# Kernel optimization log

Hardware: AMD Instinct MI355X
Metric: run time of the kernel (lower is better)

Reference implementation:

```python
import jax, jax.numpy as jnp
import numpy as np

N_NODES = 100000
N_EDGES = 1600000
N_FEAT = 128
HID = 64
HEADS = 3
CHROM = 21
N_CLASSES = 10
N_GRAPHS = 8
NEG_SLOPE = 0.2
EPS = 1e-5


def _glorot(key, shape):
    fan_in, fan_out = shape[0], shape[-1]
    lim = float(np.sqrt(6.0 / (fan_in + fan_out)))
    return jax.random.uniform(key, shape, jnp.float32, -lim, lim)


def setup_inputs() -> dict:
    key = jax.random.key(0)
    ks = jax.random.split(key, 16)
    x = jax.random.normal(ks[0], (N_NODES, N_FEAT), jnp.float32)
    src = jax.random.randint(ks[1], (N_EDGES,), 0, N_NODES)
    dst = jax.random.randint(ks[2], (N_EDGES,), 0, N_NODES)
    # avoid pre-existing self loops (PyG removes them before adding fresh ones)
    dst = jnp.where(dst == src, (dst + 1) % N_NODES, dst)
    edge_index = jnp.stack([src, dst]).astype(jnp.int64)
    batch = jnp.sort(jax.random.randint(ks[3], (N_NODES,), 0, N_GRAPHS)).astype(jnp.int64)
    d1 = HEADS * HID
    params = {
        # conv1: in 128 -> heads*64, concat=True
        'Wl1': _glorot(ks[4], (N_FEAT, d1)), 'Wr1': _glorot(ks[5], (N_FEAT, d1)),
        'att1': _glorot(ks[6], (HEADS, HID)), 'b1': jnp.zeros((d1,), jnp.float32),
        # batchnorm over 192 features
        'gamma': jnp.ones((d1,), jnp.float32), 'beta': jnp.zeros((d1,), jnp.float32),
        # conv2: in 192 -> 64 (mean over heads)
        'Wl2': _glorot(ks[7], (d1, d1)), 'Wr2': _glorot(ks[8], (d1, d1)),
        'att2': _glorot(ks[9], (HEADS, HID)), 'b2': jnp.zeros((HID,), jnp.float32),
        # conv3: in 64 -> 21 (mean over heads)
        'Wl3': _glorot(ks[10], (HID, HEADS * CHROM)), 'Wr3': _glorot(ks[11], (HID, HEADS * CHROM)),
        'att3': _glorot(ks[12], (HEADS, CHROM)), 'b3': jnp.zeros((CHROM,), jnp.float32),
        # classifier (sized to actual conv2 output width = HID)
        'Wc': _glorot(ks[13], (HID, N_CLASSES)), 'bc': jnp.zeros((N_CLASSES,), jnp.float32),
    }
    return {'x': x, 'edge_index': edge_index, 'batch': batch, **params}


def gatv2(x, src, dst, Wl, Wr, att, bias, concat):
    N = x.shape[0]
    H, D = att.shape
    xl = (x @ Wl).reshape(N, H, D)   # source transform (messages)
    xr = (x @ Wr).reshape(N, H, D)   # target transform
    e = jax.nn.leaky_relu(xl[src] + xr[dst], NEG_SLOPE)          # [E,H,D]
    logits = jnp.einsum('ehd,hd->eh', e, att)                    # [E,H]
    m = jax.ops.segment_max(logits, dst, num_segments=N)         # segment softmax over incoming edges
    ez = jnp.exp(logits - m[dst])
    z = jax.ops.segment_sum(ez, dst, num_segments=N)
    alpha = ez / z[dst]                                          # [E,H]; self-loops guarantee nonempty segments
    out = jax.ops.segment_sum(xl[src] * alpha[:, :, None], dst, num_segments=N)  # [N,H,D]
    out = out.reshape(N, H * D) if concat else out.mean(axis=1)
    return out + bias


def batchnorm(x, gamma, beta):
    mu = x.mean(axis=0)
    var = x.var(axis=0)
    return (x - mu) * jax.lax.rsqrt(var + EPS) * gamma + beta


def reference(x, edge_index, batch, Wl1, Wr1, att1, b1, gamma, beta,
              Wl2, Wr2, att2, b2, Wl3, Wr3, att3, b3, Wc, bc):
    N = x.shape[0]
    loop = jnp.arange(N, dtype=edge_index.dtype)
    src = jnp.concatenate([edge_index[0], loop])
    dst = jnp.concatenate([edge_index[1], loop])

    h = gatv2(x, src, dst, Wl1, Wr1, att1, b1, concat=True)      # [N, 192]
    h = jax.nn.relu(h)
    h = batchnorm(h, gamma, beta)
    h = gatv2(h, src, dst, Wl2, Wr2, att2, b2, concat=False)     # [N, 64]
    color = jax.nn.relu(h)
    color = gatv2(color, src, dst, Wl3, Wr3, att3, b3, concat=False)  # [N, 21]

    # global mean pool over graphs (dropout is eval-mode identity)
    sums = jax.ops.segment_sum(h, batch, num_segments=N_GRAPHS)
    cnt = jax.ops.segment_sum(jnp.ones((N, 1), h.dtype), batch, num_segments=N_GRAPHS)
    pooled = sums / jnp.maximum(cnt, 1.0)                        # [8, 64]
    classif = pooled @ Wc + bc                                   # [8, 10]
    return classif, color
```

## Files before the change

### kernel.cpp

```cpp
#include <hip/hip_runtime.h>
#include <stdint.h>
#include <math.h>

#define N_NODES 100000
#define N_EDGES 1600000
#define ETOT (N_EDGES + N_NODES)
#define NCLS 10
#define NGR 8
#define SCAN_BLOCKS ((N_NODES + 255) / 256)

typedef short v8s __attribute__((ext_vector_type(8)));
typedef float v4f __attribute__((ext_vector_type(4)));
typedef float f4v __attribute__((ext_vector_type(4)));
typedef unsigned short ushort_t;
typedef unsigned short us8 __attribute__((ext_vector_type(8)));
typedef unsigned short us4 __attribute__((ext_vector_type(4)));
typedef _Float16 h2 __attribute__((ext_vector_type(2)));
typedef _Float16 h4 __attribute__((ext_vector_type(4)));
typedef _Float16 h8 __attribute__((ext_vector_type(8)));

__device__ __forceinline__ float b2f(ushort_t u) {
    union { unsigned int i; float f; } v; v.i = ((unsigned int)u) << 16; return v.f;
}
__device__ __forceinline__ ushort_t f2b(float f) {
    union { float f; unsigned int i; } v; v.f = f;
    unsigned int u = v.i;
    unsigned int r = (u + 0x7fffu + ((u >> 16) & 1u)) >> 16;
    return (ushort_t)r;
}
__device__ __forceinline__ ushort_t f2h(float f) {
    union { _Float16 h; ushort_t u; } v; v.h = (_Float16)f; return v.u;
}

#if __has_builtin(__builtin_amdgcn_fdot2)
#define FDOT2(a, b, c) __builtin_amdgcn_fdot2((a), (b), (c), false)
#else
#define FDOT2(a, b, c) ((c) + (float)(a)[0] * (float)(b)[0] + (float)(a)[1] * (float)(b)[1])
#endif
#define SHUF2(v, i, j) __builtin_shufflevector((v), (v), (i), (j))

__device__ __forceinline__ h2 lrelu2(h2 t) {
    const h2 k = {(_Float16)0.2f, (_Float16)0.2f};
    return __builtin_elementwise_max(t, t * k);
}

__global__ void detect_kernel(const int* eidx, const unsigned int* gamma_raw,
                              int* nz, int* isf32) {
    int i = blockIdx.x * 256 + threadIdx.x;
    if (i == 0) *isf32 = (gamma_raw[0] == 0x3F800000u) ? 1 : 0;
    if (eidx[2 * i + 1] != 0) atomicAdd(nz, 1);
}

struct CArgs {
    const void* src[10];
    ushort_t*   dst[10];
    int         len[10];
    int         tohalf[10];
};
__global__ void convert_small(CArgs c, const int* isf32) {
    int seg = blockIdx.x;
    int f32 = *isf32;
    int th = c.tohalf[seg];
    for (int i = threadIdx.x; i < c.len[seg]; i += 256) {
        float v = f32 ? ((const float*)c.src[seg])[i] : b2f(((const ushort_t*)c.src[seg])[i]);
        c.dst[seg][i] = th ? f2h(v) : f2b(v);
    }
}

struct TArgs {
    const void* W[6];
    ushort_t*   Wt[6];
    int K[6], Nn[6], Kp[6], Np[6];
    int bstart[7];
};
__global__ void transpose_all(TArgs t, const int* isf32) {
    int b = blockIdx.x;
    int seg = 0;
    while (seg < 5 && b >= t.bstart[seg + 1]) seg++;
    int i = (b - t.bstart[seg]) * 256 + threadIdx.x;
    int Kp = t.Kp[seg];
    if (i >= t.Np[seg] * Kp) return;
    int n = i / Kp, k = i - n * Kp;
    ushort_t v = 0;
    if (n < t.Nn[seg] && k < t.K[seg]) {
        long idx = (long)k * t.Nn[seg] + n;
        v = (*isf32) ? f2b(((const float*)t.W[seg])[idx]) : ((const ushort_t*)t.W[seg])[idx];
    }
    t.Wt[seg][i] = v;
}

__global__ void hist_kernel(const int* eidx, const int* nz, int* counts) {
    long i = (long)blockIdx.x * 256 + threadIdx.x;
    if (i >= ETOT) return;
    int w64 = (*nz == 0);
    int d;
    if (i < N_EDGES) d = w64 ? eidx[2 * (N_EDGES + i)] : eidx[N_EDGES + i];
    else             d = (int)(i - N_EDGES);
    if ((unsigned)d >= N_NODES) d = 0;
    atomicAdd(&counts[d], 1);
}

__global__ void scan_part(const int* counts, int* blocksum) {
    __shared__ int red[256];
    int i = blockIdx.x * 256 + threadIdx.x;
    int v = (i < N_NODES) ? counts[i] : 0;
    red[threadIdx.x] = v;
    __syncthreads();
    for (int off = 128; off > 0; off >>= 1) {
        if (threadIdx.x < off) red[threadIdx.x] += red[threadIdx.x + off];
        __syncthreads();
    }
    if (threadIdx.x == 0) blocksum[blockIdx.x] = red[0];
}

__global__ void scan_top(int* blocksum) {
    __shared__ int part[512];
    int t = threadIdx.x;
    int v = (t < SCAN_BLOCKS) ? blocksum[t] : 0;
    part[t] = v;
    __syncthreads();
    for (int off = 1; off < 512; off <<= 1) {
        int x = part[t];
        int add = (t >= off) ? part[t - off] : 0;
        __syncthreads();
        part[t] = x + add;
        __syncthreads();
    }
    if (t < SCAN_BLOCKS) blocksum[t] = part[t] - v;
}

__global__ void scan_final(const int* counts, const int* blocksum, int* row_ptr) {
    __shared__ int part[256];
    int i = blockIdx.x * 256 + threadIdx.x;
    int v = (i < N_NODES) ? counts[i] : 0;
    part[threadIdx.x] = v;
    __syncthreads();
    for (int off = 1; off < 256; off <<= 1) {
        int x = part[threadIdx.x];
        int add = (threadIdx.x >= off) ? part[threadIdx.x - off] : 0;
        __syncthreads();
        part[threadIdx.x] = x + add;
        __syncthreads();
    }
    int incl = part[threadIdx.x];
    int base = blocksum[blockIdx.x];
    if (i < N_NODES) row_ptr[i] = base + incl - v;
    if (i == N_NODES - 1) row_ptr[N_NODES] = base + incl;
}

__global__ void scatter_kernel(const int* eidx, const int* nz, const int* row_ptr,
                               int* cursor, int* csr) {
    long i = (long)blockIdx.x * 256 + threadIdx.x;
    if (i >= ETOT) return;
    int w64 = (*nz == 0);
    int s, d;
    if (i < N_EDGES) {
        s = w64 ? eidx[2 * i] : eidx[i];
        d = w64 ? eidx[2 * (N_EDGES + i)] : eidx[N_EDGES + i];
    } else { s = d = (int)(i - N_EDGES); }
    if ((unsigned)s >= N_NODES) s = 0;
    if ((unsigned)d >= N_NODES) d = 0;
    int pos = atomicAdd(&cursor[d], 1);
    csr[row_ptr[d] + pos] = s;
}

template <int K, int MODE>
__global__ void gemm_dual_pack(const void* A, const short* W1t, const short* W2t,
                               ushort_t* O1A, ushort_t* O1B, ushort_t* O2A, ushort_t* O2B,
                               int srcauto, const float* scale, const float* shift,
                               const int* isf32) {
    constexpr int KITERS = K / 32;
    constexpr int NTILES = MODE ? 12 : 4;
    __shared__ ushort_t atile[32 * K];
    int tid = threadIdx.x;
    int f32src = srcauto && (*isf32);
    constexpr int CPR = K / 8;
    size_t nodeBase = (size_t)blockIdx.x * 32;

    for (int c = tid; c < 32 * CPR; c += 256) {
        int row = c / CPR, kc = c - row * CPR;
        size_t node = nodeBase + row;
        ushort_t tmp[8];
        if (f32src) {
            const f4v* src = (const f4v*)((const float*)A + node * K + kc * 8);
            f4v v0 = src[0], v1 = src[1];
            #pragma unroll
            for (int j = 0; j < 4; j++) { tmp[j] = f2b(v0[j]); tmp[4 + j] = f2b(v1[j]); }
        } else {
            us8 v = *(const us8*)((const ushort_t*)A + node * K + kc * 8);
            #pragma unroll
            for (int j = 0; j < 8; j++) tmp[j] = v[j];
        }
        if (scale) {
            #pragma unroll
            for (int j = 0; j < 8; j++)
                tmp[j] = f2b(b2f(tmp[j]) * scale[kc * 8 + j] + shift[kc * 8 + j]);
        }
        int ki = kc >> 2, q = kc & 3;
        *(us8*)&atile[((ki * 32 + row) * 4 + q) * 8] = *(us8*)tmp;
    }
    __syncthreads();

    int wave = tid >> 6, lane = tid & 63;
    int rw = lane & 15, q = lane >> 4;

    v8s afr[2][KITERS];
    #pragma unroll
    for (int m = 0; m < 2; m++)
        #pragma unroll
        for (int ki = 0; ki < KITERS; ki++)
            afr[m][ki] = *(const v8s*)&atile[((ki * 32 + m * 16 + rw) * 4 + q) * 8];

    for (int nt = wave; nt < NTILES; nt += 4) {
        const short* b1p = W1t + (size_t)(nt * 16 + rw) * K + q * 8;
        const short* b2p = W2t + (size_t)(nt * 16 + rw) * K + q * 8;
        v4f c1[2] = {{0,0,0,0},{0,0,0,0}}, c2[2] = {{0,0,0,0},{0,0,0,0}};
        #pragma unroll
        for (int ki = 0; ki < KITERS; ki++) {
            v8s b1 = *(const v8s*)(b1p + ki * 32);
            v8s b2 = *(const v8s*)(b2p + ki * 32);
            c1[0] = __builtin_amdgcn_mfma_f32_16x16x32_bf16(afr[0][ki], b1, c1[0], 0, 0, 0);
            c1[1] = __builtin_amdgcn_mfma_f32_16x16x32_bf16(afr[1][ki], b1, c1[1], 0, 0, 0);
            c2[0] = __builtin_amdgcn_mfma_f32_16x16x32_bf16(afr[0][ki], b2, c2[0], 0, 0, 0);
            c2[1] = __builtin_amdgcn_mfma_f32_16x16x32_bf16(afr[1][ki], b2, c2[1], 0, 0, 0);
        }
        int cn = nt * 16 + rw;
        #pragma unroll
        for (int m = 0; m < 2; m++) {
            if (MODE) {
                int h = cn >> 6, d = cn & 63;
                int l = d >> 2, k = d & 3;
                #pragma unroll
                for (int r = 0; r < 4; r++) {
                    size_t node = nodeBase + m * 16 + q * 4 + r;
                    if (h < 2) {
                        size_t ad = (node * 16 + l) * 8 + h * 4 + k;
                        O1A[ad] = f2h(c1[m][r]); O2A[ad] = f2h(c2[m][r]);
                    } else {
                        size_t ad = (node * 16 + l) * 4 + k;
                        O1B[ad] = f2h(c1[m][r]); O2B[ad] = f2h(c2[m][r]);
                    }
                }
            } else if (cn < 63) {
                int h = cn / 21, d = cn - h * 21;
                int l = d & 15, k = d >> 4;
                #pragma unroll
                for (int r = 0; r < 4; r++) {
                    size_t node = nodeBase + m * 16 + q * 4 + r;
                    size_t ad = (node * 16 + l) * 8 + h * 2 + k;
                    O1A[ad] = f2h(c1[m][r]); O2A[ad] = f2h(c2[m][r]);
                }
            }
        }
    }
}

__global__ void edge_fused_192(const ushort_t* __restrict__ xlA_, const ushort_t* __restrict__ xlB_,
                               const ushort_t* __restrict__ xrA_, const ushort_t* __restrict__ xrB_,
                               const ushort_t* __restrict__ att_, const int* __restrict__ row_ptr,
                               const int* __restrict__ csr, const ushort_t* bias, int mode,
                               ushort_t* out_a, ushort_t* out_b) {
    const _Float16* xlA = (const _Float16*)xlA_;
    const _Float16* xlB = (const _Float16*)xlB_;
    const _Float16* xrA = (const _Float16*)xrA_;
    const _Float16* xrB = (const _Float16*)xrB_;
    const _Float16* att = (const _Float16*)att_;
    int wid = blockIdx.x * 4 + (threadIdx.x >> 6);
    int lane = threadIdx.x & 63;
    size_t n = wid;
    int quad = lane >> 4, l = lane & 15;

    h8 rv8 = *(const h8*)(xrA + (n * 16 + l) * 8);
    h4 rv4 = *(const h4*)(xrB + (n * 16 + l) * 4);
    h4 av0 = *(const h4*)(att + 4 * l);
    h4 av1 = *(const h4*)(att + 64 + 4 * l);
    h4 av2 = *(const h4*)(att + 128 + 4 * l);
    h2 rp0 = SHUF2(rv8, 0, 1), rp1 = SHUF2(rv8, 2, 3);
    h2 rp2 = SHUF2(rv8, 4, 5), rp3 = SHUF2(rv8, 6, 7);
    h2 rp4 = SHUF2(rv4, 0, 1), rp5 = SHUF2(rv4, 2, 3);
    h2 ap0 = SHUF2(av0, 0, 1), ap1 = SHUF2(av0, 2, 3);
    h2 ap2 = SHUF2(av1, 0, 1), ap3 = SHUF2(av1, 2, 3);
    h2 ap4 = SHUF2(av2, 0, 1), ap5 = SHUF2(av2, 2, 3);

    float z0 = 0.f, z1 = 0.f, z2 = 0.f;
    float A[12];
    #pragma unroll
    for (int k = 0; k < 12; k++) A[k] = 0.f;

    int beg = row_ptr[n], end = row_ptr[n + 1];
    for (int chunk = beg; chunk < end; chunk += 64) {
        int cnt = end - chunk; if (cnt > 64) cnt = 64;
        int sv = csr[chunk + (lane < cnt ? lane : cnt - 1)];
        for (int jj = 0; jj < cnt; jj += 4) {
            int j = jj + quad;
            int act = j < cnt;
            int jc = act ? j : cnt - 1;
            size_t s = (size_t)__shfl(sv, jc, 64);
            h8 xv8 = *(const h8*)(xlA + (s * 16 + l) * 8);
            h4 xv4 = *(const h4*)(xlB + (s * 16 + l) * 4);
            float p0 = FDOT2(ap0, lrelu2(SHUF2(xv8, 0, 1) + rp0), 0.f);
            p0 = FDOT2(ap1, lrelu2(SHUF2(xv8, 2, 3) + rp1), p0);
            float p1 = FDOT2(ap2, lrelu2(SHUF2(xv8, 4, 5) + rp2), 0.f);
            p1 = FDOT2(ap3, lrelu2(SHUF2(xv8, 6, 7) + rp3), p1);
            float p2 = FDOT2(ap4, lrelu2(SHUF2(xv4, 0, 1) + rp4), 0.f);
            p2 = FDOT2(ap5, lrelu2(SHUF2(xv4, 2, 3) + rp5), p2);
            #pragma unroll
            for (int o = 8; o > 0; o >>= 1) {
                p0 += __shfl_xor(p0, o, 64);
                p1 += __shfl_xor(p1, o, 64);
                p2 += __shfl_xor(p2, o, 64);
            }
            float e0 = act ? __expf(p0) : 0.f;
            float e1 = act ? __expf(p1) : 0.f;
            float e2 = act ? __expf(p2) : 0.f;
            z0 += e0; z1 += e1; z2 += e2;
            #pragma unroll
            for (int k = 0; k < 4; k++) {
                A[k]     = fmaf((float)xv8[k],     e0, A[k]);
                A[4 + k] = fmaf((float)xv8[4 + k], e1, A[4 + k]);
                A[8 + k] = fmaf((float)xv4[k],     e2, A[8 + k]);
            }
        }
    }

    #pragma unroll
    for (int st = 16; st <= 32; st <<= 1) {
        z0 += __shfl_xor(z0, st, 64);
        z1 += __shfl_xor(z1, st, 64);
        z2 += __shfl_xor(z2, st, 64);
        #pragma unroll
        for (int k = 0; k < 12; k++) A[k] += __shfl_xor(A[k], st, 64);
    }

    if (quad == 0) {
        float i0 = 1.f / z0, i1 = 1.f / z1, i2 = 1.f / z2;
        if (mode == 1) {
            ushort_t o0[4], o1[4], o2[4];
            #pragma unroll
            for (int k = 0; k < 4; k++) {
                o0[k] = f2b(fmaxf(A[k] * i0 + b2f(bias[4 * l + k]), 0.f));
                o1[k] = f2b(fmaxf(A[4 + k] * i1 + b2f(bias[64 + 4 * l + k]), 0.f));
                o2[k] = f2b(fmaxf(A[8 + k] * i2 + b2f(bias[128 + 4 * l + k]), 0.f));
            }
            *(uint2*)(out_a + n * 192 + 4 * l) = *(uint2*)o0;
            *(uint2*)(out_a + n * 192 + 64 + 4 * l) = *(uint2*)o1;
            *(uint2*)(out_a + n * 192 + 128 + 4 * l) = *(uint2*)o2;
        } else {
            ushort_t oh[4], oc[4];
            #pragma unroll
            for (int k = 0; k < 4; k++) {
                float hv = (A[k] * i0 + A[4 + k] * i1 + A[8 + k] * i2) * (1.0f / 3.0f)
                           + b2f(bias[4 * l + k]);
                oh[k] = f2b(hv);
                oc[k] = f2b(fmaxf(hv, 0.f));
            }
            *(uint2*)(out_a + n * 64 + 4 * l) = *(uint2*)oh;
            *(uint2*)(out_b + n * 64 + 4 * l) = *(uint2*)oc;
        }
    }
}

__global__ void edge_fused_63(const ushort_t* __restrict__ xlA_, const ushort_t* __restrict__ xrA_,
                              const ushort_t* __restrict__ att_, const int* __restrict__ row_ptr,
                              const int* __restrict__ csr, const ushort_t* bias,
                              void* dout, const int* isf32) {
    const _Float16* xlA = (const _Float16*)xlA_;
    const _Float16* xrA = (const _Float16*)xrA_;
    const _Float16* att = (const _Float16*)att_;
    int wid = blockIdx.x * 4 + (threadIdx.x >> 6);
    int lane = threadIdx.x & 63;
    size_t n = wid;
    int quad = lane >> 4, l = lane & 15;
    int k1ok = (l < 5);
    const _Float16 HZ = (_Float16)0.f;

    h8 rv = *(const h8*)(xrA + (n * 16 + l) * 8);
    h2 rp[3], ap[3];
    #pragma unroll
    for (int h = 0; h < 3; h++) {
        rp[h][0] = rv[h * 2];
        rp[h][1] = k1ok ? rv[h * 2 + 1] : HZ;
        ap[h][0] = att[h * 21 + l];
        ap[h][1] = k1ok ? att[h * 21 + 16 + l] : HZ;
    }
    float z0 = 0.f, z1 = 0.f, z2 = 0.f;
    float A[6];
    #pragma unroll
    for (int k = 0; k < 6; k++) A[k] = 0.f;

    int beg = row_ptr[n], end = row_ptr[n + 1];
    for (int chunk = beg; chunk < end; chunk += 64) {
        int cnt = end - chunk; if (cnt > 64) cnt = 64;
        int sv = csr[chunk + (lane < cnt ? lane : cnt - 1)];
        for (int jj = 0; jj < cnt; jj += 4) {
            int j = jj + quad;
            int act = j < cnt;
            int jc = act ? j : cnt - 1;
            size_t s = (size_t)__shfl(sv, jc, 64);
            h8 xv = *(const h8*)(xlA + (s * 16 + l) * 8);
            h2 xp[3];
            #pragma unroll
            for (int h = 0; h < 3; h++) {
                xp[h][0] = xv[h * 2];
                xp[h][1] = k1ok ? xv[h * 2 + 1] : HZ;
            }
            float p0 = FDOT2(ap[0], lrelu2(xp[0] + rp[0]), 0.f);
            float p1 = FDOT2(ap[1], lrelu2(xp[1] + rp[1]), 0.f);
            float p2 = FDOT2(ap[2], lrelu2(xp[2] + rp[2]), 0.f);
            #pragma unroll
            for (int o = 8; o > 0; o >>= 1) {
                p0 += __shfl_xor(p0, o, 64);
                p1 += __shfl_xor(p1, o, 64);
                p2 += __shfl_xor(p2, o, 64);
            }
            float e0 = act ? __expf(p0) : 0.f;
            float e1 = act ? __expf(p1) : 0.f;
            float e2 = act ? __expf(p2) : 0.f;
            z0 += e0; z1 += e1; z2 += e2;
            A[0] = fmaf((float)xp[0][0], e0, A[0]);
            A[1] = fmaf((float)xp[0][1], e0, A[1]);
            A[2] = fmaf((float)xp[1][0], e1, A[2]);
            A[3] = fmaf((float)xp[1][1], e1, A[3]);
            A[4] = fmaf((float)xp[2][0], e2, A[4]);
            A[5] = fmaf((float)xp[2][1], e2, A[5]);
        }
    }

    #pragma unroll
    for (int st = 16; st <= 32; st <<= 1) {
        z0 += __shfl_xor(z0, st, 64);
        z1 += __shfl_xor(z1, st, 64);
        z2 += __shfl_xor(z2, st, 64);
        #pragma unroll
        for (int k = 0; k < 6; k++) A[k] += __shfl_xor(A[k], st, 64);
    }

    if (quad == 0) {
        float i0 = 1.f / z0, i1 = 1.f / z1, i2 = 1.f / z2;
        float o0 = (A[0] * i0 + A[2] * i1 + A[4] * i2) * (1.0f / 3.0f) + b2f(bias[l]);
        size_t oi = 80 + n * 21 + l;
        int f32 = *isf32;
        if (f32) ((float*)dout)[oi] = o0;
        else     ((ushort_t*)dout)[oi] = f2b(o0);
        if (k1ok) {
            float o1 = (A[1] * i0 + A[3] * i1 + A[5] * i2) * (1.0f / 3.0f)
                       + b2f(bias[16 + l]);
            size_t oj = 80 + n * 21 + 16 + l;
            if (f32) ((float*)dout)[oj] = o1;
            else     ((ushort_t*)dout)[oj] = f2b(o1);
        }
    }
}

__global__ void bn_stats(const ushort_t* h, float* sum, float* sq) {
    int j = threadIdx.x;
    long r0 = (long)blockIdx.x * 256;
    float s = 0.f, q = 0.f;
    for (int i = 0; i < 256; i++) {
        long r = r0 + i;
        if (r >= N_NODES) break;
        float v = b2f(h[r * 192 + j]);
        s += v; q += v * v;
    }
    atomicAdd(&sum[j], s); atomicAdd(&sq[j], q);
}

__global__ void bn_finalize(const float* sum, const float* sq, const ushort_t* gamma,
                            const ushort_t* beta, float* scale, float* shift) {
    int j = threadIdx.x;
    if (j >= 192) return;
    float mu = sum[j] / (float)N_NODES;
    float var = sq[j] / (float)N_NODES - mu * mu;
    float inv = rsqrtf(fmaxf(var, 0.f) + 1e-5f);
    float sc = b2f(gamma[j]) * inv;
    scale[j] = sc;
    shift[j] = b2f(beta[j]) - mu * sc;
}

__global__ void pool_accum(const ushort_t* h2, const int* batchp, const int* nz,
                           float* psum, float* pcnt) {
    __shared__ float ls[NGR * 64];
    __shared__ float lc[NGR];
    for (int i = threadIdx.x; i < NGR * 64; i += blockDim.x) ls[i] = 0.f;
    if (threadIdx.x < NGR) lc[threadIdx.x] = 0.f;
    __syncthreads();
    int w64 = (*nz == 0);
    int f = threadIdx.x & 63;
    int rr = threadIdx.x >> 6;
    long r0 = (long)blockIdx.x * 1024;
    long rend = r0 + 1024; if (rend > N_NODES) rend = N_NODES;
    for (long r = r0 + rr; r < rend; r += 4) {
        int g = w64 ? batchp[2 * r] : batchp[r];
        g &= 7;
        atomicAdd(&ls[g * 64 + f], b2f(h2[r * 64 + f]));
        if (f == 0) atomicAdd(&lc[g], 1.0f);
    }
    __syncthreads();
    for (int i = threadIdx.x; i < NGR * 64; i += blockDim.x) atomicAdd(&psum[i], ls[i]);
    if (threadIdx.x < NGR) atomicAdd(&pcnt[threadIdx.x], lc[threadIdx.x]);
}

__global__ void classifier(const float* psum, const float* pcnt, const ushort_t* Wc,
                           const ushort_t* bc, void* dout, const int* isf32) {
    int i = threadIdx.x;
    if (i >= NGR * NCLS) return;
    int g = i / NCLS, c = i - g * NCLS;
    float cnt = fmaxf(pcnt[g], 1.0f);
    float s = 0.f;
    for (int d = 0; d < 64; d++)
        s += (psum[g * 64 + d] / cnt) * b2f(Wc[d * NCLS + c]);
    float o = s + b2f(bc[c]);
    if (*isf32) ((float*)dout)[i] = o;
    else        ((ushort_t*)dout)[i] = f2b(o);
}

extern "C" void kernel_launch(void* const* d_in, const int* in_sizes, int n_in,
                              void* d_out, int out_size, void* d_ws, size_t ws_size,
                              hipStream_t stream) {
    const void* x_raw   = d_in[0];
    const int*  eidx    = (const int*)d_in[1];
    const int*  batch   = (const int*)d_in[2];
    const void* Wl1     = d_in[3];
    const void* Wr1     = d_in[4];
    const void* att1r   = d_in[5];
    const void* b1r     = d_in[6];
    const void* gammar  = d_in[7];
    const void* betar   = d_in[8];
    const void* Wl2     = d_in[9];
    const void* Wr2     = d_in[10];
    const void* att2r   = d_in[11];
    const void* b2r     = d_in[12];
    const void* Wl3     = d_in[13];
    const void* Wr3     = d_in[14];
    const void* att3r   = d_in[15];
    const void* b3r     = d_in[16];
    const void* Wcr     = d_in[17];
    const void* bcr     = d_in[18];

    char* w = (char*)d_ws;
    size_t off = 0;
    auto alloc = [&](size_t bytes) -> char* {
        char* p = w + off;
        off = (off + bytes + 255) & ~(size_t)255;
        return p;
    };

    size_t meta_beg = off;
    int*   nz      = (int*)alloc(4);
    int*   isf32   = (int*)alloc(4);
    int*   counts  = (int*)alloc(4 * (size_t)N_NODES);
    int*   cursor  = (int*)alloc(4 * (size_t)N_NODES);
    float* bn_sum  = (float*)alloc(4 * 192);
    float* bn_sq   = (float*)alloc(4 * 192);
    float* psum    = (float*)alloc(4 * NGR * 64);
    float* pcnt    = (float*)alloc(4 * NGR);
    size_t meta_bytes = off - meta_beg;

    float* bn_scale = (float*)alloc(4 * 192);
    float* bn_shift = (float*)alloc(4 * 192);
    int*   blocksum = (int*)alloc(4 * 512);
    int*   row_ptr  = (int*)alloc(4 * (size_t)(N_NODES + 1));
    int*   csr      = (int*)alloc(4 * (size_t)ETOT);
    ushort_t* xlpA  = (ushort_t*)alloc(2 * (size_t)N_NODES * 128);
    ushort_t* xrpA  = (ushort_t*)alloc(2 * (size_t)N_NODES * 128);
    ushort_t* xlpB  = (ushort_t*)alloc(2 * (size_t)N_NODES * 64);
    ushort_t* xrpB  = (ushort_t*)alloc(2 * (size_t)N_NODES * 64);
    ushort_t* regC  = (ushort_t*)alloc(2 * (size_t)N_NODES * 192);
    ushort_t* hbn    = regC;
    ushort_t* h2v    = regC;
    ushort_t* colorb = regC + (size_t)N_NODES * 64;
    ushort_t* wt1l  = (ushort_t*)alloc(2 * 192 * 128);
    ushort_t* wt1r  = (ushort_t*)alloc(2 * 192 * 128);
    ushort_t* wt2l  = (ushort_t*)alloc(2 * 192 * 192);
    ushort_t* wt2r  = (ushort_t*)alloc(2 * 192 * 192);
    ushort_t* wt3l  = (ushort_t*)alloc(2 * 64 * 64);
    ushort_t* wt3r  = (ushort_t*)alloc(2 * 64 * 64);
    ushort_t* att1c = (ushort_t*)alloc(2 * 192);
    ushort_t* att2c = (ushort_t*)alloc(2 * 192);
    ushort_t* att3c = (ushort_t*)alloc(2 * 64);
    ushort_t* b1c   = (ushort_t*)alloc(2 * 192);
    ushort_t* b2c   = (ushort_t*)alloc(2 * 64);
    ushort_t* b3c   = (ushort_t*)alloc(2 * 32);
    ushort_t* gamc  = (ushort_t*)alloc(2 * 192);
    ushort_t* betc  = (ushort_t*)alloc(2 * 192);
    ushort_t* Wcc   = (ushort_t*)alloc(2 * 640);
    ushort_t* bcc   = (ushort_t*)alloc(2 * 16);
    (void)ws_size; (void)in_sizes; (void)n_in; (void)out_size;

    hipMemsetAsync(w + meta_beg, 0, meta_bytes, stream);

    detect_kernel<<<256, 256, 0, stream>>>(eidx, (const unsigned int*)gammar, nz, isf32);

    {
        CArgs c;
        const void* s[10] = {att1r, att2r, att3r, b1r, b2r, b3r, gammar, betar, Wcr, bcr};
        ushort_t* d[10]   = {att1c, att2c, att3c, b1c, b2c, b3c, gamc,  betc,  Wcc, bcc};
        int ln[10]        = {192,   192,   63,    192, 64,  21,  192,   192,   640, 10};
        int th[10]        = {1,     1,     1,     0,   0,   0,   0,     0,     0,   0};
        for (int i = 0; i < 10; i++) {
            c.src[i] = s[i]; c.dst[i] = d[i]; c.len[i] = ln[i]; c.tohalf[i] = th[i];
        }
        convert_small<<<10, 256, 0, stream>>>(c, isf32);
    }

    {
        TArgs t;
        const void* s[6] = {Wl1, Wr1, Wl2, Wr2, Wl3, Wr3};
        ushort_t* d[6]   = {wt1l, wt1r, wt2l, wt2r, wt3l, wt3r};
        int K[6]  = {128, 128, 192, 192, 64, 64};
        int Nn[6] = {192, 192, 192, 192, 63, 63};
        int Kp[6] = {128, 128, 192, 192, 64, 64};
        int Np[6] = {192, 192, 192, 192, 64, 64};
        int bs = 0;
        for (int i = 0; i < 6; i++) {
            t.W[i] = s[i]; t.Wt[i] = d[i];
            t.K[i] = K[i]; t.Nn[i] = Nn[i]; t.Kp[i] = Kp[i]; t.Np[i] = Np[i];
            t.bstart[i] = bs;
            bs += (Np[i] * Kp[i] + 255) / 256;
        }
        t.bstart[6] = bs;
        transpose_all<<<bs, 256, 0, stream>>>(t, isf32);
    }

    hist_kernel<<<(ETOT + 255) / 256, 256, 0, stream>>>(eidx, nz, counts);
    scan_part<<<SCAN_BLOCKS, 256, 0, stream>>>(counts, blocksum);
    scan_top<<<1, 512, 0, stream>>>(blocksum);
    scan_final<<<SCAN_BLOCKS, 256, 0, stream>>>(counts, blocksum, row_ptr);
    scatter_kernel<<<(ETOT + 255) / 256, 256, 0, stream>>>(eidx, nz, row_ptr, cursor, csr);

    const int nodeBlocks = N_NODES / 4;
    const int gemmBlocks = N_NODES / 32;

    gemm_dual_pack<128, 1><<<gemmBlocks, 256, 0, stream>>>(
        x_raw, (const short*)wt1l, (const short*)wt1r,
        xlpA, xlpB, xrpA, xrpB, 1, nullptr, nullptr, isf32);
    edge_fused_192<<<nodeBlocks, 256, 0, stream>>>(xlpA, xlpB, xrpA, xrpB, att1c,
                                                   row_ptr, csr, b1c, 1, hbn, hbn);

    bn_stats<<<(N_NODES + 255) / 256, 192, 0, stream>>>(hbn, bn_sum, bn_sq);
    bn_finalize<<<1, 192, 0, stream>>>(bn_sum, bn_sq, gamc, betc, bn_scale, bn_shift);

    gemm_dual_pack<192, 1><<<gemmBlocks, 256, 0, stream>>>(
        hbn, (const short*)wt2l, (const short*)wt2r,
        xlpA, xlpB, xrpA, xrpB, 0, bn_scale, bn_shift, isf32);
    edge_fused_192<<<nodeBlocks, 256, 0, stream>>>(xlpA, xlpB, xrpA, xrpB, att2c,
                                                   row_ptr, csr, b2c, 2, h2v, colorb);

    pool_accum<<<(N_NODES + 1023) / 1024, 256, 0, stream>>>(h2v, batch, nz, psum, pcnt);

    gemm_dual_pack<64, 0><<<gemmBlocks, 256, 0, stream>>>(
        colorb, (const short*)wt3l, (const short*)wt3r,
        xlpA, xlpB, xrpA, xrpB, 0, nullptr, nullptr, isf32);
    edge_fused_63<<<nodeBlocks, 256, 0, stream>>>(xlpA, xrpA, att3c, row_ptr, csr, b3c,
                                                  d_out, isf32);

    classifier<<<1, 128, 0, stream>>>(psum, pcnt, Wcc, bcc, d_out, isf32);
}
```

Before: 937.9 us.

## Process nodes in descending-degree order and compact layer-3 feature packing

Adds a counting sort of nodes by in-degree (histogram into the scan, a bin scan, and a scatter into a permutation). The edge kernels then process nodes highest-degree first, meant to reduce tail imbalance across waves. Layer 3 packs its 63 features as 4 contiguous halves per lane instead of an 8-wide padded layout, halving gather bytes per edge. The cost is a per-element head select plus an LDS reduction across heads at the output, and the scattered node order may hurt locality of output writes and row_ptr reads.

Result: slower. 1.500 ms (+60.0%).

```diff
diff --git a/kernel.cpp b/kernel.cpp
--- a/kernel.cpp
+++ b/kernel.cpp
@@ -129,7 +129,8 @@
     if (t < SCAN_BLOCKS) blocksum[t] = part[t] - v;
 }
 
-__global__ void scan_final(const int* counts, const int* blocksum, int* row_ptr) {
+__global__ void scan_final(const int* counts, const int* blocksum, int* row_ptr,
+                           int* degbin) {
     __shared__ int part[256];
     int i = blockIdx.x * 256 + threadIdx.x;
     int v = (i < N_NODES) ? counts[i] : 0;
@@ -144,8 +145,37 @@
     }
     int incl = part[threadIdx.x];
     int base = blocksum[blockIdx.x];
-    if (i < N_NODES) row_ptr[i] = base + incl - v;
+    if (i < N_NODES) {
+        row_ptr[i] = base + incl - v;
+        int bin = v > 1023 ? 1023 : v;
+        atomicAdd(&degbin[bin], 1);
+    }
     if (i == N_NODES - 1) row_ptr[N_NODES] = base + incl;
+}
+
+__global__ void dsort_scan(int* degbin) {
+    __shared__ int part[1024];
+    int t = threadIdx.x;
+    int v = degbin[t];
+    part[t] = v;
+    __syncthreads();
+    for (int off = 1; off < 1024; off <<= 1) {
+        int x = part[t];
+        int add = (t >= off) ? part[t - off] : 0;
+        __syncthreads();
+        part[t] = x + add;
+        __syncthreads();
+    }
+    degbin[t] = part[t] - v;
+}
+
+__global__ void dsort_scatter(const int* counts, const int* degbase, int* degcur,
+                              int* perm) {
+    int i = blockIdx.x * 256 + threadIdx.x;
+    if (i >= N_NODES) return;
+    int bin = counts[i]; if (bin > 1023) bin = 1023;
+    int pos = atomicAdd(&degcur[bin], 1);
+    perm[degbase[bin] + pos] = i;
 }
 
 __global__ void scatter_kernel(const int* eidx, const int* nz, const int* row_ptr,
@@ -242,12 +272,11 @@
                     }
                 }
             } else if (cn < 63) {
-                int h = cn / 21, d = cn - h * 21;
-                int l = d & 15, k = d >> 4;
+                int l = cn >> 2, k = cn & 3;
                 #pragma unroll
                 for (int r = 0; r < 4; r++) {
                     size_t node = nodeBase + m * 16 + q * 4 + r;
-                    size_t ad = (node * 16 + l) * 8 + h * 2 + k;
+                    size_t ad = (node * 16 + l) * 4 + k;
                     O1A[ad] = f2h(c1[m][r]); O2A[ad] = f2h(c2[m][r]);
                 }
             }
@@ -258,7 +287,8 @@
 __global__ void edge_fused_192(const ushort_t* __restrict__ xlA_, const ushort_t* __restrict__ xlB_,
                                const ushort_t* __restrict__ xrA_, const ushort_t* __restrict__ xrB_,
                                const ushort_t* __restrict__ att_, const int* __restrict__ row_ptr,
-                               const int* __restrict__ csr, const ushort_t* bias, int mode,
+                               const int* __restrict__ csr, const int* __restrict__ perm,
+                               const ushort_t* bias, int mode,
                                ushort_t* out_a, ushort_t* out_b) {
     const _Float16* xlA = (const _Float16*)xlA_;
     const _Float16* xlB = (const _Float16*)xlB_;
@@ -267,7 +297,7 @@
     const _Float16* att = (const _Float16*)att_;
     int wid = blockIdx.x * 4 + (threadIdx.x >> 6);
     int lane = threadIdx.x & 63;
-    size_t n = wid;
+    size_t n = (size_t)perm[N_NODES - 1 - wid];
     int quad = lane >> 4, l = lane & 15;
 
     h8 rv8 = *(const h8*)(xrA + (n * 16 + l) * 8);
@@ -360,33 +390,39 @@
     }
 }
 
-__global__ void edge_fused_63(const ushort_t* __restrict__ xlA_, const ushort_t* __restrict__ xrA_,
+__global__ void edge_fused_63(const ushort_t* __restrict__ xl_, const ushort_t* __restrict__ xr_,
                               const ushort_t* __restrict__ att_, const int* __restrict__ row_ptr,
-                              const int* __restrict__ csr, const ushort_t* bias,
-                              void* dout, const int* isf32) {
-    const _Float16* xlA = (const _Float16*)xlA_;
-    const _Float16* xrA = (const _Float16*)xrA_;
+                              const int* __restrict__ csr, const int* __restrict__ perm,
+                              const ushort_t* bias, void* dout, const int* isf32) {
+    const _Float16* xl = (const _Float16*)xl_;
+    const _Float16* xr = (const _Float16*)xr_;
     const _Float16* att = (const _Float16*)att_;
-    int wid = blockIdx.x * 4 + (threadIdx.x >> 6);
+    __shared__ float ls[4 * 64];
+    int wave = threadIdx.x >> 6;
+    int wid = blockIdx.x * 4 + wave;
     int lane = threadIdx.x & 63;
-    size_t n = wid;
+    size_t n = (size_t)perm[N_NODES - 1 - wid];
     int quad = lane >> 4, l = lane & 15;
-    int k1ok = (l < 5);
-    const _Float16 HZ = (_Float16)0.f;
-
-    h8 rv = *(const h8*)(xrA + (n * 16 + l) * 8);
-    h2 rp[3], ap[3];
+    int f0 = 4 * l;
+
+    h2 ah[3][2];
     #pragma unroll
-    for (int h = 0; h < 3; h++) {
-        rp[h][0] = rv[h * 2];
-        rp[h][1] = k1ok ? rv[h * 2 + 1] : HZ;
-        ap[h][0] = att[h * 21 + l];
-        ap[h][1] = k1ok ? att[h * 21 + 16 + l] : HZ;
-    }
+    for (int h = 0; h < 3; h++)
+        #pragma unroll
+        for (int p = 0; p < 2; p++) {
+            int fa = f0 + 2 * p, fb = fa + 1;
+            ah[h][p][0] = (fa < 63 && fa / 21 == h) ? att[fa] : (_Float16)0.f;
+            ah[h][p][1] = (fb < 63 && fb / 21 == h) ? att[fb] : (_Float16)0.f;
+        }
+    bool b21[4], b42[4];
+    #pragma unroll
+    for (int k = 0; k < 4; k++) { b21[k] = (f0 + k) < 21; b42[k] = (f0 + k) < 42; }
+
+    h4 rv = *(const h4*)(xr + (n * 16 + l) * 4);
+    h2 r01 = SHUF2(rv, 0, 1), r23 = SHUF2(rv, 2, 3);
+
     float z0 = 0.f, z1 = 0.f, z2 = 0.f;
-    float A[6];
-    #pragma unroll
-    for (int k = 0; k < 6; k++) A[k] = 0.f;
+    float A[4] = {0.f, 0.f, 0.f, 0.f};
 
     int beg = row_ptr[n], end = row_ptr[n + 1];
     for (int chunk = beg; chunk < end; chunk += 64) {
@@ -397,16 +433,12 @@
             int act = j < cnt;
             int jc = act ? j : cnt - 1;
             size_t s = (size_t)__shfl(sv, jc, 64);
-            h8 xv = *(const h8*)(xlA + (s * 16 + l) * 8);
-            h2 xp[3];
-            #pragma unroll
-            for (int h = 0; h < 3; h++) {
-                xp[h][0] = xv[h * 2];
-                xp[h][1] = k1ok ? xv[h * 2 + 1] : HZ;
-            }
-            float p0 = FDOT2(ap[0], lrelu2(xp[0] + rp[0]), 0.f);
-            float p1 = FDOT2(ap[1], lrelu2(xp[1] + rp[1]), 0.f);
-            float p2 = FDOT2(ap[2], lrelu2(xp[2] + rp[2]), 0.f);
+            h4 xv = *(const h4*)(xl + (s * 16 + l) * 4);
+            h2 x01 = SHUF2(xv, 0, 1), x23 = SHUF2(xv, 2, 3);
+            h2 t01 = lrelu2(x01 + r01), t23 = lrelu2(x23 + r23);
+            float p0 = FDOT2(ah[0][1], t23, FDOT2(ah[0][0], t01, 0.f));
+            float p1 = FDOT2(ah[1][1], t23, FDOT2(ah[1][0], t01, 0.f));
+            float p2 = FDOT2(ah[2][1], t23, FDOT2(ah[2][0], t01, 0.f));
             #pragma unroll
             for (int o = 8; o > 0; o >>= 1) {
                 p0 += __shfl_xor(p0, o, 64);
@@ -417,12 +449,11 @@
             float e1 = act ? __expf(p1) : 0.f;
             float e2 = act ? __expf(p2) : 0.f;
             z0 += e0; z1 += e1; z2 += e2;
-            A[0] = fmaf((float)xp[0][0], e0, A[0]);
-            A[1] = fmaf((float)xp[0][1], e0, A[1]);
-            A[2] = fmaf((float)xp[1][0], e1, A[2]);
-            A[3] = fmaf((float)xp[1][1], e1, A[3]);
-            A[4] = fmaf((float)xp[2][0], e2, A[4]);
-            A[5] = fmaf((float)xp[2][1], e2, A[5]);
+            #pragma unroll
+            for (int k = 0; k < 4; k++) {
+                float ek = b21[k] ? e0 : (b42[k] ? e1 : e2);
+                A[k] = fmaf((float)xv[k], ek, A[k]);
+            }
         }
     }
 
@@ -432,23 +463,24 @@
         z1 += __shfl_xor(z1, st, 64);
         z2 += __shfl_xor(z2, st, 64);
         #pragma unroll
-        for (int k = 0; k < 6; k++) A[k] += __shfl_xor(A[k], st, 64);
+        for (int k = 0; k < 4; k++) A[k] += __shfl_xor(A[k], st, 64);
     }
 
     if (quad == 0) {
         float i0 = 1.f / z0, i1 = 1.f / z1, i2 = 1.f / z2;
-        float o0 = (A[0] * i0 + A[2] * i1 + A[4] * i2) * (1.0f / 3.0f) + b2f(bias[l]);
-        size_t oi = 80 + n * 21 + l;
-        int f32 = *isf32;
-        if (f32) ((float*)dout)[oi] = o0;
-        else     ((ushort_t*)dout)[oi] = f2b(o0);
-        if (k1ok) {
-            float o1 = (A[1] * i0 + A[3] * i1 + A[5] * i2) * (1.0f / 3.0f)
-                       + b2f(bias[16 + l]);
-            size_t oj = 80 + n * 21 + 16 + l;
-            if (f32) ((float*)dout)[oj] = o1;
-            else     ((ushort_t*)dout)[oj] = f2b(o1);
-        }
+        #pragma unroll
+        for (int k = 0; k < 4; k++) {
+            float iv = b21[k] ? i0 : (b42[k] ? i1 : i2);
+            ls[wave * 64 + f0 + k] = A[k] * iv;
+        }
+    }
+    __syncthreads();
+    if (lane < 21) {
+        float o = (ls[wave * 64 + lane] + ls[wave * 64 + 21 + lane]
+                   + ls[wave * 64 + 42 + lane]) * (1.0f / 3.0f) + b2f(bias[lane]);
+        size_t oi = 80 + n * 21 + lane;
+        if (*isf32) ((float*)dout)[oi] = o;
+        else        ((ushort_t*)dout)[oi] = f2b(o);
     }
 }
 
@@ -550,6 +582,8 @@
     int*   isf32   = (int*)alloc(4);
     int*   counts  = (int*)alloc(4 * (size_t)N_NODES);
     int*   cursor  = (int*)alloc(4 * (size_t)N_NODES);
+    int*   degbin  = (int*)alloc(4 * 1024);
+    int*   degcur  = (int*)alloc(4 * 1024);
     float* bn_sum  = (float*)alloc(4 * 192);
     float* bn_sq   = (float*)alloc(4 * 192);
     float* psum    = (float*)alloc(4 * NGR * 64);
@@ -560,6 +594,7 @@
     float* bn_shift = (float*)alloc(4 * 192);
     int*   blocksum = (int*)alloc(4 * 512);
     int*   row_ptr  = (int*)alloc(4 * (size_t)(N_NODES + 1));
+    int*   perm     = (int*)alloc(4 * (size_t)N_NODES);
     int*   csr      = (int*)alloc(4 * (size_t)ETOT);
     ushort_t* xlpA  = (ushort_t*)alloc(2 * (size_t)N_NODES * 128);
     ushort_t* xrpA  = (ushort_t*)alloc(2 * (size_t)N_NODES * 128);
@@ -625,7 +660,9 @@
     hist_kernel<<<(ETOT + 255) / 256, 256, 0, stream>>>(eidx, nz, counts);
     scan_part<<<SCAN_BLOCKS, 256, 0, stream>>>(counts, blocksum);
     scan_top<<<1, 512, 0, stream>>>(blocksum);
-    scan_final<<<SCAN_BLOCKS, 256, 0, stream>>>(counts, blocksum, row_ptr);
+    scan_final<<<SCAN_BLOCKS, 256, 0, stream>>>(counts, blocksum, row_ptr, degbin);
+    dsort_scan<<<1, 1024, 0, stream>>>(degbin);
+    dsort_scatter<<<SCAN_BLOCKS, 256, 0, stream>>>(counts, degbin, degcur, perm);
     scatter_kernel<<<(ETOT + 255) / 256, 256, 0, stream>>>(eidx, nz, row_ptr, cursor, csr);
 
     const int nodeBlocks = N_NODES / 4;
@@ -635,7 +672,7 @@
         x_raw, (const short*)wt1l, (const short*)wt1r,
         xlpA, xlpB, xrpA, xrpB, 1, nullptr, nullptr, isf32);
     edge_fused_192<<<nodeBlocks, 256, 0, stream>>>(xlpA, xlpB, xrpA, xrpB, att1c,
-                                                   row_ptr, csr, b1c, 1, hbn, hbn);
+                                                   row_ptr, csr, perm, b1c, 1, hbn, hbn);
 
     bn_stats<<<(N_NODES + 255) / 256, 192, 0, stream>>>(hbn, bn_sum, bn_sq);
     bn_finalize<<<1, 192, 0, stream>>>(bn_sum, bn_sq, gamc, betc, bn_scale, bn_shift);
@@ -644,15 +681,15 @@
         hbn, (const short*)wt2l, (const short*)wt2r,
         xlpA, xlpB, xrpA, xrpB, 0, bn_scale, bn_shift, isf32);
     edge_fused_192<<<nodeBlocks, 256, 0, stream>>>(xlpA, xlpB, xrpA, xrpB, att2c,
-                                                   row_ptr, csr, b2c, 2, h2v, colorb);
+                                                   row_ptr, csr, perm, b2c, 2, h2v, colorb);
 
     pool_accum<<<(N_NODES + 1023) / 1024, 256, 0, stream>>>(h2v, batch, nz, psum, pcnt);
 
     gemm_dual_pack<64, 0><<<gemmBlocks, 256, 0, stream>>>(
         colorb, (const short*)wt3l, (const short*)wt3r,
         xlpA, xlpB, xrpA, xrpB, 0, nullptr, nullptr, isf32);
-    edge_fused_63<<<nodeBlocks, 256, 0, stream>>>(xlpA, xrpA, att3c, row_ptr, csr, b3c,
-                                                  d_out, isf32);
+    edge_fused_63<<<nodeBlocks, 256, 0, stream>>>(xlpA, xrpA, att3c, row_ptr, csr, perm,
+                                                  b3c, d_out, isf32);
 
     classifier<<<1, 128, 0, stream>>>(psum, pcnt, Wcc, bcc, d_out, isf32);
 }
```
